# Kernel tuning notes

Measured on AMD Instinct MI355X. Metric: run time of the kernel, lower is better.

Reference implementation:

```python
import jax, jax.numpy as jnp
import numpy as np

VOCAB = 50000
EMBED = 128
CONTENT = 200
HIDDEN = 1024
LABELS = 2
BATCH = 4096


def setup_inputs() -> dict:
    key = jax.random.key(0)
    k_x, k_emb, k_w1, k_b1, k_w2, k_b2 = jax.random.split(key, 6)
    x = jax.random.randint(k_x, (BATCH, CONTENT), 0, VOCAB, dtype=jnp.int64)
    emb_table = jax.random.normal(k_emb, (VOCAB, EMBED), dtype=jnp.float32)
    fan_in1 = EMBED * CONTENT
    w1 = jax.random.uniform(k_w1, (HIDDEN, fan_in1), dtype=jnp.float32,
                            minval=-1.0, maxval=1.0) / np.sqrt(fan_in1)
    b1 = jax.random.uniform(k_b1, (HIDDEN,), dtype=jnp.float32,
                            minval=-1.0, maxval=1.0) / np.sqrt(fan_in1)
    w2 = jax.random.uniform(k_w2, (LABELS, HIDDEN), dtype=jnp.float32,
                            minval=-1.0, maxval=1.0) / np.sqrt(HIDDEN)
    b2 = jax.random.uniform(k_b2, (LABELS,), dtype=jnp.float32,
                            minval=-1.0, maxval=1.0) / np.sqrt(HIDDEN)
    return {"x": x, "emb_table": emb_table, "w1": w1, "b1": b1,
            "w2": w2, "b2": b2}


def reference(x, emb_table, w1, b1, w2, b2):
    # padding_idx=0: row 0 of the embedding table is zero
    table = emb_table.at[0].set(0.0)
    emb = table[x]                                   # [B, C, E]
    flat = emb.reshape(emb.shape[0], -1)             # [B, C*E]
    h = jax.nn.relu(flat @ w1.T + b1)                # [B, H]
    logits = h @ w2.T + b2                           # [B, L]
    # Softmax(dim=0) on a 1-D per-sample vector == softmax over labels
    return jax.nn.softmax(logits, axis=-1)
```

## Files before the change

kernel.cpp:

```cpp
#include <hip/hip_runtime.h>
#include <hip/hip_bf16.h>
#include <stdint.h>

#define BATCH   4096
#define CONTENT 200
#define EMBED   128
#define HIDDEN  1024
#define KDIM    (CONTENT*EMBED)
#define KSTEPS64 (KDIM/64)
#define SPLITK  3
#define KCHUNK64 134

typedef __bf16 bf16_t;
typedef __bf16 bf16x8 __attribute__((ext_vector_type(8)));
typedef float  f32x4  __attribute__((ext_vector_type(4)));

#define WS_EMBT  0ull
#define WS_W1    12800000ull
#define WS_HP    65228800ull
#define HP_STRIDE 4194304ull

__device__ __forceinline__ void gload_lds16(const void* g, void* l) {
  __builtin_amdgcn_global_load_lds(
      (const __attribute__((address_space(1))) uint32_t*)g,
      (__attribute__((address_space(3))) uint32_t*)l, 16, 0, 0);
}

__global__ __launch_bounds__(256) void k_cast_emb(const float* __restrict__ emb,
                                                  bf16_t* __restrict__ o) {
  const int NU = 50000 * EMBED / 8;
  int stride = gridDim.x * 256;
  for (int u = blockIdx.x * 256 + threadIdx.x; u < NU; u += stride) {
    const float4* s = (const float4*)(emb + (size_t)u * 8);
    float4 f0 = s[0], f1 = s[1];
    float sc = (u >> 4) == 0 ? 0.0f : 1.0f;
    bf16x8 r;
    r[0]=(bf16_t)(f0.x*sc); r[1]=(bf16_t)(f0.y*sc); r[2]=(bf16_t)(f0.z*sc); r[3]=(bf16_t)(f0.w*sc);
    r[4]=(bf16_t)(f1.x*sc); r[5]=(bf16_t)(f1.y*sc); r[6]=(bf16_t)(f1.z*sc); r[7]=(bf16_t)(f1.w*sc);
    *(bf16x8*)(o + (size_t)u * 8) = r;
  }
}

__global__ __launch_bounds__(256) void k_cast_w1(const float* __restrict__ w1,
                                                 bf16_t* __restrict__ o) {
  const long long NU = (long long)HIDDEN * KDIM / 8;
  long long stride = (long long)gridDim.x * 256;
  for (long long u = (long long)blockIdx.x * 256 + threadIdx.x; u < NU; u += stride) {
    const float4* s = (const float4*)(w1 + u * 8);
    float4 f0 = s[0], f1 = s[1];
    bf16x8 r;
    r[0]=(bf16_t)f0.x; r[1]=(bf16_t)f0.y; r[2]=(bf16_t)f0.z; r[3]=(bf16_t)f0.w;
    r[4]=(bf16_t)f1.x; r[5]=(bf16_t)f1.y; r[6]=(bf16_t)f1.z; r[7]=(bf16_t)f1.w;
    *(bf16x8*)(o + u * 8) = r;
  }
}

__global__ __launch_bounds__(256) void k_gemm(const int* __restrict__ x,
                                              const bf16_t* __restrict__ embT,
                                              const bf16_t* __restrict__ W,
                                              float* __restrict__ hp) {
  __shared__ char smem[32768];
  const int tid = threadIdx.x;
  const int w = tid >> 6, l = tid & 63;
  const int m0 = blockIdx.x * 128;
  const int n0 = blockIdx.y * 128;
  const int chunk = blockIdx.z;
  const int ks_begin = chunk * KCHUNK64;
  int ks_end = ks_begin + KCHUNK64; if (ks_end > KSTEPS64) ks_end = KSTEPS64;

  const int rbase = tid >> 3;
  const int sg = (tid & 7) ^ (rbase & 7);
  const char* embB = (const char*)embT;
  const char* Wb = (const char*)W;
  char* dstA0 = smem + w * 1024;
  char* dstB0 = smem + 16384 + w * 1024;

  const char* bsrc[4];
  #pragma unroll
  for (int rd = 0; rd < 4; ++rd)
    bsrc[rd] = Wb + (size_t)(n0 + rd * 32 + rbase) * (KDIM * 2)
                  + (size_t)ks_begin * 128 + sg * 16;

  int c = ks_begin >> 1;
  int xv[4], xvn[4];
  #pragma unroll
  for (int rd = 0; rd < 4; ++rd)
    xv[rd] = x[(m0 + rd * 32 + rbase) * CONTENT + c];
  {
    int cn = c + 1; if (cn > CONTENT - 1) cn = CONTENT - 1;
    #pragma unroll
    for (int rd = 0; rd < 4; ++rd)
      xvn[rd] = x[(m0 + rd * 32 + rbase) * CONTENT + cn];
  }

  const int wr = w >> 1, wc = w & 1;
  const int lane_r = l & 15;
  const int g = l >> 4;
  const char* AsB = smem;
  const char* BsB = smem + 16384;

  f32x4 acc[4][4];
  #pragma unroll
  for (int i = 0; i < 4; ++i)
    #pragma unroll
    for (int j = 0; j < 4; ++j)
      acc[i][j] = (f32x4){0.f, 0.f, 0.f, 0.f};

  for (int ks = ks_begin; ks < ks_end; ++ks) {
    if ((ks & 1) == 0 && ks > ks_begin) {
      ++c;
      #pragma unroll
      for (int rd = 0; rd < 4; ++rd) xv[rd] = xvn[rd];
      int cn = c + 1; if (cn > CONTENT - 1) cn = CONTENT - 1;
      #pragma unroll
      for (int rd = 0; rd < 4; ++rd)
        xvn[rd] = x[(m0 + rd * 32 + rbase) * CONTENT + cn];
    }
    const int koffA = (ks & 1) << 7;
    #pragma unroll
    for (int rd = 0; rd < 4; ++rd) {
      gload_lds16(embB + (size_t)xv[rd] * 256 + koffA + sg * 16,
                  dstA0 + rd * 4096);
      gload_lds16(bsrc[rd], dstB0 + rd * 4096);
      bsrc[rd] += 128;
    }
    __syncthreads();

    #pragma unroll
    for (int kk = 0; kk < 2; ++kk) {
      bf16x8 af[4], bfr[4];
      #pragma unroll
      for (int i = 0; i < 4; ++i) {
        int rowa = wr * 64 + i * 16 + lane_r;
        int rowb = wc * 64 + i * 16 + lane_r;
        int slot = ((kk << 2) | g) ^ (lane_r & 7);
        af[i]  = *(const bf16x8*)(AsB + rowa * 128 + slot * 16);
        bfr[i] = *(const bf16x8*)(BsB + rowb * 128 + slot * 16);
      }
      #pragma unroll
      for (int i = 0; i < 4; ++i)
        #pragma unroll
        for (int j = 0; j < 4; ++j)
          acc[i][j] = __builtin_amdgcn_mfma_f32_16x16x32_bf16(af[i], bfr[j], acc[i][j], 0, 0, 0);
    }
    __syncthreads();
  }

  float* hout = hp + (size_t)chunk * HP_STRIDE;
  const int colBase = n0 + wc * 64 + lane_r;
  const int rowBase = m0 + wr * 64 + (l >> 4) * 4;
  #pragma unroll
  for (int i = 0; i < 4; ++i)
    #pragma unroll
    for (int j = 0; j < 4; ++j)
      #pragma unroll
      for (int r = 0; r < 4; ++r)
        hout[(size_t)(rowBase + i * 16 + r) * HIDDEN + colBase + j * 16] = acc[i][j][r];
}

__global__ __launch_bounds__(256) void k_final(const float* __restrict__ hp,
                                               const float* __restrict__ b1,
                                               const float* __restrict__ w2,
                                               const float* __restrict__ b2,
                                               float* __restrict__ out) {
  const int tid = threadIdx.x;
  const int w = tid >> 6, l = tid & 63;
  const int m = blockIdx.x * 4 + w;
  const float* r0 = hp + (size_t)m * HIDDEN;
  const float* r1 = r0 + HP_STRIDE;
  const float* r2 = r1 + HP_STRIDE;
  float l0 = 0.f, l1 = 0.f;
  #pragma unroll
  for (int t = 0; t < 4; ++t) {
    int j = t * 256 + l * 4;
    float4 p0 = *(const float4*)(r0 + j);
    float4 p1 = *(const float4*)(r1 + j);
    float4 p2 = *(const float4*)(r2 + j);
    float4 bb = *(const float4*)(b1 + j);
    float4 wa = *(const float4*)(w2 + j);
    float4 wb = *(const float4*)(w2 + HIDDEN + j);
    float h;
    h = p0.x + p1.x + p2.x + bb.x; h = fmaxf(h, 0.f); l0 += h * wa.x; l1 += h * wb.x;
    h = p0.y + p1.y + p2.y + bb.y; h = fmaxf(h, 0.f); l0 += h * wa.y; l1 += h * wb.y;
    h = p0.z + p1.z + p2.z + bb.z; h = fmaxf(h, 0.f); l0 += h * wa.z; l1 += h * wb.z;
    h = p0.w + p1.w + p2.w + bb.w; h = fmaxf(h, 0.f); l0 += h * wa.w; l1 += h * wb.w;
  }
  #pragma unroll
  for (int off = 32; off > 0; off >>= 1) {
    l0 += __shfl_xor(l0, off, 64);
    l1 += __shfl_xor(l1, off, 64);
  }
  if (l == 0) {
    float z0 = l0 + b2[0], z1 = l1 + b2[1];
    float mx = fmaxf(z0, z1);
    float e0 = expf(z0 - mx), e1 = expf(z1 - mx);
    float s = 1.f / (e0 + e1);
    out[2 * m]     = e0 * s;
    out[2 * m + 1] = e1 * s;
  }
}

extern "C" void kernel_launch(void* const* d_in, const int* in_sizes, int n_in,
                              void* d_out, int out_size, void* d_ws, size_t ws_size,
                              hipStream_t stream) {
  (void)in_sizes; (void)n_in; (void)out_size; (void)ws_size;
  const int*   x   = (const int*)d_in[0];
  const float* emb = (const float*)d_in[1];
  const float* w1  = (const float*)d_in[2];
  const float* b1  = (const float*)d_in[3];
  const float* w2  = (const float*)d_in[4];
  const float* b2  = (const float*)d_in[5];
  float* out = (float*)d_out;
  char* ws = (char*)d_ws;
  bf16_t* embT = (bf16_t*)(ws + WS_EMBT);
  bf16_t* Wbf  = (bf16_t*)(ws + WS_W1);
  float*  hp   = (float*)(ws + WS_HP);

  hipLaunchKernelGGL(k_cast_emb, dim3(1024), dim3(256), 0, stream, emb, embT);
  hipLaunchKernelGGL(k_cast_w1,  dim3(2048), dim3(256), 0, stream, w1, Wbf);
  hipLaunchKernelGGL(k_gemm,     dim3(BATCH/128, HIDDEN/128, SPLITK), dim3(256), 0, stream,
                     x, embT, Wbf, hp);
  hipLaunchKernelGGL(k_final,    dim3(BATCH/4), dim3(256), 0, stream, hp, b1, w2, b2, out);
}
```

Baseline: 421.2 us.

## Double-buffer GEMM LDS tiles, cut split-K to two, merge cast kernels

The GEMM main loop now keeps two LDS stages (64KB). Loads for step t+2 are issued right after the barrier that ends step t, so global-to-LDS gathers overlap MFMA work, and the per-step barriers drop from two to one. Split-K goes from 3 to 2 chunks of 200 steps, which means fewer partial-sum writes and reads in the final reduction. The two fp32-to-bf16 cast kernels are merged into one launch, and s_setprio is raised around the MFMA block. Doubling LDS lowers occupancy, and the smaller split-K grid launches fewer blocks.

```diff
diff --git a/kernel.cpp b/kernel.cpp
--- a/kernel.cpp
+++ b/kernel.cpp
@@ -8,8 +8,8 @@
 #define HIDDEN  1024
 #define KDIM    (CONTENT*EMBED)
 #define KSTEPS64 (KDIM/64)
-#define SPLITK  3
-#define KCHUNK64 134
+#define SPLITK  2
+#define KCHUNK64 200
 
 typedef __bf16 bf16_t;
 typedef __bf16 bf16x8 __attribute__((ext_vector_type(8)));
@@ -26,32 +26,33 @@
       (__attribute__((address_space(3))) uint32_t*)l, 16, 0, 0);
 }
 
-__global__ __launch_bounds__(256) void k_cast_emb(const float* __restrict__ emb,
-                                                  bf16_t* __restrict__ o) {
-  const int NU = 50000 * EMBED / 8;
-  int stride = gridDim.x * 256;
-  for (int u = blockIdx.x * 256 + threadIdx.x; u < NU; u += stride) {
-    const float4* s = (const float4*)(emb + (size_t)u * 8);
-    float4 f0 = s[0], f1 = s[1];
-    float sc = (u >> 4) == 0 ? 0.0f : 1.0f;
-    bf16x8 r;
-    r[0]=(bf16_t)(f0.x*sc); r[1]=(bf16_t)(f0.y*sc); r[2]=(bf16_t)(f0.z*sc); r[3]=(bf16_t)(f0.w*sc);
-    r[4]=(bf16_t)(f1.x*sc); r[5]=(bf16_t)(f1.y*sc); r[6]=(bf16_t)(f1.z*sc); r[7]=(bf16_t)(f1.w*sc);
-    *(bf16x8*)(o + (size_t)u * 8) = r;
-  }
-}
-
-__global__ __launch_bounds__(256) void k_cast_w1(const float* __restrict__ w1,
-                                                 bf16_t* __restrict__ o) {
-  const long long NU = (long long)HIDDEN * KDIM / 8;
-  long long stride = (long long)gridDim.x * 256;
-  for (long long u = (long long)blockIdx.x * 256 + threadIdx.x; u < NU; u += stride) {
-    const float4* s = (const float4*)(w1 + u * 8);
-    float4 f0 = s[0], f1 = s[1];
-    bf16x8 r;
-    r[0]=(bf16_t)f0.x; r[1]=(bf16_t)f0.y; r[2]=(bf16_t)f0.z; r[3]=(bf16_t)f0.w;
-    r[4]=(bf16_t)f1.x; r[5]=(bf16_t)f1.y; r[6]=(bf16_t)f1.z; r[7]=(bf16_t)f1.w;
-    *(bf16x8*)(o + u * 8) = r;
+__global__ __launch_bounds__(256) void k_prep(const float* __restrict__ emb,
+                                              const float* __restrict__ w1,
+                                              bf16_t* __restrict__ embT,
+                                              bf16_t* __restrict__ w1T) {
+  if (blockIdx.x < 320) {
+    const int NU = 800000;
+    int stride = 320 * 256;
+    for (int u = blockIdx.x * 256 + threadIdx.x; u < NU; u += stride) {
+      const float4* s = (const float4*)(emb + (size_t)u * 8);
+      float4 f0 = s[0], f1 = s[1];
+      float sc = (u >> 4) == 0 ? 0.0f : 1.0f;
+      bf16x8 r;
+      r[0]=(bf16_t)(f0.x*sc); r[1]=(bf16_t)(f0.y*sc); r[2]=(bf16_t)(f0.z*sc); r[3]=(bf16_t)(f0.w*sc);
+      r[4]=(bf16_t)(f1.x*sc); r[5]=(bf16_t)(f1.y*sc); r[6]=(bf16_t)(f1.z*sc); r[7]=(bf16_t)(f1.w*sc);
+      *(bf16x8*)(embT + (size_t)u * 8) = r;
+    }
+  } else {
+    const long long NU = 3276800;
+    long long stride = 2048LL * 256;
+    for (long long u = (long long)(blockIdx.x - 320) * 256 + threadIdx.x; u < NU; u += stride) {
+      const float4* s = (const float4*)(w1 + u * 8);
+      float4 f0 = s[0], f1 = s[1];
+      bf16x8 r;
+      r[0]=(bf16_t)f0.x; r[1]=(bf16_t)f0.y; r[2]=(bf16_t)f0.z; r[3]=(bf16_t)f0.w;
+      r[4]=(bf16_t)f1.x; r[5]=(bf16_t)f1.y; r[6]=(bf16_t)f1.z; r[7]=(bf16_t)f1.w;
+      *(bf16x8*)(w1T + u * 8) = r;
+    }
   }
 }
 
@@ -59,21 +60,19 @@
                                               const bf16_t* __restrict__ embT,
                                               const bf16_t* __restrict__ W,
                                               float* __restrict__ hp) {
-  __shared__ char smem[32768];
+  __shared__ char smem[65536];
   const int tid = threadIdx.x;
   const int w = tid >> 6, l = tid & 63;
   const int m0 = blockIdx.x * 128;
   const int n0 = blockIdx.y * 128;
   const int chunk = blockIdx.z;
   const int ks_begin = chunk * KCHUNK64;
-  int ks_end = ks_begin + KCHUNK64; if (ks_end > KSTEPS64) ks_end = KSTEPS64;
+  const int nt = KCHUNK64;
 
   const int rbase = tid >> 3;
   const int sg = (tid & 7) ^ (rbase & 7);
   const char* embB = (const char*)embT;
   const char* Wb = (const char*)W;
-  char* dstA0 = smem + w * 1024;
-  char* dstB0 = smem + 16384 + w * 1024;
 
   const char* bsrc[4];
   #pragma unroll
@@ -81,23 +80,27 @@
     bsrc[rd] = Wb + (size_t)(n0 + rd * 32 + rbase) * (KDIM * 2)
                   + (size_t)ks_begin * 128 + sg * 16;
 
-  int c = ks_begin >> 1;
-  int xv[4], xvn[4];
+  int tokc = ks_begin >> 1;
+  int xv[4], xn[4];
   #pragma unroll
   for (int rd = 0; rd < 4; ++rd)
-    xv[rd] = x[(m0 + rd * 32 + rbase) * CONTENT + c];
-  {
-    int cn = c + 1; if (cn > CONTENT - 1) cn = CONTENT - 1;
-    #pragma unroll
-    for (int rd = 0; rd < 4; ++rd)
-      xvn[rd] = x[(m0 + rd * 32 + rbase) * CONTENT + cn];
-  }
+    xv[rd] = x[(m0 + rd * 32 + rbase) * CONTENT + tokc];
+  #pragma unroll
+  for (int rd = 0; rd < 4; ++rd)
+    xn[rd] = x[(m0 + rd * 32 + rbase) * CONTENT + tokc + 1];
+
+#define ISSUE(koff, base)                                                     \
+  { _Pragma("unroll")                                                         \
+    for (int rd = 0; rd < 4; ++rd) {                                          \
+      gload_lds16(embB + (size_t)xv[rd] * 256 + (koff) + sg * 16,             \
+                  smem + (base) + w * 1024 + rd * 4096);                      \
+      gload_lds16(bsrc[rd], smem + (base) + 16384 + w * 1024 + rd * 4096);    \
+      bsrc[rd] += 128;                                                        \
+    } }
 
   const int wr = w >> 1, wc = w & 1;
   const int lane_r = l & 15;
   const int g = l >> 4;
-  const char* AsB = smem;
-  const char* BsB = smem + 16384;
 
   f32x4 acc[4][4];
   #pragma unroll
@@ -106,25 +109,13 @@
     for (int j = 0; j < 4; ++j)
       acc[i][j] = (f32x4){0.f, 0.f, 0.f, 0.f};
 
-  for (int ks = ks_begin; ks < ks_end; ++ks) {
-    if ((ks & 1) == 0 && ks > ks_begin) {
-      ++c;
-      #pragma unroll
-      for (int rd = 0; rd < 4; ++rd) xv[rd] = xvn[rd];
-      int cn = c + 1; if (cn > CONTENT - 1) cn = CONTENT - 1;
-      #pragma unroll
-      for (int rd = 0; rd < 4; ++rd)
-        xvn[rd] = x[(m0 + rd * 32 + rbase) * CONTENT + cn];
-    }
-    const int koffA = (ks & 1) << 7;
-    #pragma unroll
-    for (int rd = 0; rd < 4; ++rd) {
-      gload_lds16(embB + (size_t)xv[rd] * 256 + koffA + sg * 16,
-                  dstA0 + rd * 4096);
-      gload_lds16(bsrc[rd], dstB0 + rd * 4096);
-      bsrc[rd] += 128;
-    }
-    __syncthreads();
+  ISSUE(0, 0);
+  ISSUE(128, 32768);
+  __syncthreads();
+
+  for (int t = 0; t < nt; ++t) {
+    const char* AsB = smem + ((t & 1) << 15);
+    const char* BsB = AsB + 16384;
 
     #pragma unroll
     for (int kk = 0; kk < 2; ++kk) {
@@ -137,14 +128,33 @@
         af[i]  = *(const bf16x8*)(AsB + rowa * 128 + slot * 16);
         bfr[i] = *(const bf16x8*)(BsB + rowb * 128 + slot * 16);
       }
+      __builtin_amdgcn_s_setprio(1);
       #pragma unroll
       for (int i = 0; i < 4; ++i)
         #pragma unroll
         for (int j = 0; j < 4; ++j)
           acc[i][j] = __builtin_amdgcn_mfma_f32_16x16x32_bf16(af[i], bfr[j], acc[i][j], 0, 0, 0);
-    }
+      __builtin_amdgcn_s_setprio(0);
+    }
+
     __syncthreads();
-  }
+
+    int tt = t + 2;
+    if (tt < nt) {
+      int ks = ks_begin + tt;
+      if ((ks & 1) == 0) {
+        tokc = ks >> 1;
+        #pragma unroll
+        for (int rd = 0; rd < 4; ++rd) xv[rd] = xn[rd];
+        int nxt = tokc + 1; if (nxt > CONTENT - 1) nxt = CONTENT - 1;
+        #pragma unroll
+        for (int rd = 0; rd < 4; ++rd)
+          xn[rd] = x[(m0 + rd * 32 + rbase) * CONTENT + nxt];
+      }
+      ISSUE((ks & 1) << 7, (t & 1) << 15);
+    }
+  }
+#undef ISSUE
 
   float* hout = hp + (size_t)chunk * HP_STRIDE;
   const int colBase = n0 + wc * 64 + lane_r;
@@ -168,22 +178,20 @@
   const int m = blockIdx.x * 4 + w;
   const float* r0 = hp + (size_t)m * HIDDEN;
   const float* r1 = r0 + HP_STRIDE;
-  const float* r2 = r1 + HP_STRIDE;
   float l0 = 0.f, l1 = 0.f;
   #pragma unroll
   for (int t = 0; t < 4; ++t) {
     int j = t * 256 + l * 4;
     float4 p0 = *(const float4*)(r0 + j);
     float4 p1 = *(const float4*)(r1 + j);
-    float4 p2 = *(const float4*)(r2 + j);
     float4 bb = *(const float4*)(b1 + j);
     float4 wa = *(const float4*)(w2 + j);
     float4 wb = *(const float4*)(w2 + HIDDEN + j);
     float h;
-    h = p0.x + p1.x + p2.x + bb.x; h = fmaxf(h, 0.f); l0 += h * wa.x; l1 += h * wb.x;
-    h = p0.y + p1.y + p2.y + bb.y; h = fmaxf(h, 0.f); l0 += h * wa.y; l1 += h * wb.y;
-    h = p0.z + p1.z + p2.z + bb.z; h = fmaxf(h, 0.f); l0 += h * wa.z; l1 += h * wb.z;
-    h = p0.w + p1.w + p2.w + bb.w; h = fmaxf(h, 0.f); l0 += h * wa.w; l1 += h * wb.w;
+    h = p0.x + p1.x + bb.x; h = fmaxf(h, 0.f); l0 += h * wa.x; l1 += h * wb.x;
+    h = p0.y + p1.y + bb.y; h = fmaxf(h, 0.f); l0 += h * wa.y; l1 += h * wb.y;
+    h = p0.z + p1.z + bb.z; h = fmaxf(h, 0.f); l0 += h * wa.z; l1 += h * wb.z;
+    h = p0.w + p1.w + bb.w; h = fmaxf(h, 0.f); l0 += h * wa.w; l1 += h * wb.w;
   }
   #pragma unroll
   for (int off = 32; off > 0; off >>= 1) {
@@ -216,9 +224,8 @@
   bf16_t* Wbf  = (bf16_t*)(ws + WS_W1);
   float*  hp   = (float*)(ws + WS_HP);
 
-  hipLaunchKernelGGL(k_cast_emb, dim3(1024), dim3(256), 0, stream, emb, embT);
-  hipLaunchKernelGGL(k_cast_w1,  dim3(2048), dim3(256), 0, stream, w1, Wbf);
-  hipLaunchKernelGGL(k_gemm,     dim3(BATCH/128, HIDDEN/128, SPLITK), dim3(256), 0, stream,
+  hipLaunchKernelGGL(k_prep,  dim3(2368), dim3(256), 0, stream, emb, w1, embT, Wbf);
+  hipLaunchKernelGGL(k_gemm,  dim3(BATCH/128, HIDDEN/128, SPLITK), dim3(256), 0, stream,
                      x, embT, Wbf, hp);
-  hipLaunchKernelGGL(k_final,    dim3(BATCH/4), dim3(256), 0, stream, hp, b1, w2, b2, out);
-}
+  hipLaunchKernelGGL(k_final, dim3(BATCH/4), dim3(256), 0, stream, hp, b1, w2, b2, out);
+}
```

New measurement: 435.0 us. 3.3% more time.
